# Performance work log

Hardware: AMD Instinct MI355X
Metric: run time of the kernel (lower is better)

## Reference

```python
import jax, jax.numpy as jnp
import numpy as np

N_NODES = 16384
K_NBR = 16
N_HOPS = 4  # hops + 2
IN_DIM = 256
RAW_DIM = 128
OUT_DIM = 64
PHI_DIM = 16
N_KERN = 4
E = N_NODES * K_NBR


def setup_inputs() -> dict:
    key = jax.random.key(0)
    ks = jax.random.split(key, 16)
    s = 0.05  # small weight scale for numerical sanity
    h = jax.random.normal(ks[0], (N_NODES, IN_DIM), jnp.float32)
    e_tensor = jax.random.normal(ks[1], (N_HOPS, N_NODES, RAW_DIM), jnp.float32)
    # kNN-style edges: each dst node has exactly K_NBR incoming edges
    src = jax.random.randint(ks[2], (N_HOPS, E), 0, N_NODES, jnp.int32)
    dst = jnp.tile(jnp.repeat(jnp.arange(N_NODES, dtype=jnp.int32), K_NBR)[None, :], (N_HOPS, 1))
    return {
        'h': h,
        'e_tensor': e_tensor,
        'src': src,
        'dst': dst,
        'W_phi': jax.random.normal(ks[3], (N_HOPS, RAW_DIM, PHI_DIM - 1), jnp.float32) * s,
        'mlp_w1': jax.random.normal(ks[4], (N_HOPS, RAW_DIM, IN_DIM), jnp.float32) * s,
        'mlp_b1': jax.random.normal(ks[5], (N_HOPS, IN_DIM), jnp.float32) * s,
        'mlp_w2': jax.random.normal(ks[6], (N_HOPS, IN_DIM, PHI_DIM * N_KERN), jnp.float32) * s,
        'mlp_b2': jax.random.normal(ks[7], (N_HOPS, PHI_DIM * N_KERN), jnp.float32) * s,
        'tilde_phi': jax.random.normal(ks[8], (N_HOPS, N_KERN, PHI_DIM), jnp.float32),
        'W': jax.random.normal(ks[9], (N_HOPS, IN_DIM, OUT_DIM * N_KERN), jnp.float32) * s,
        'bias': jax.random.normal(ks[10], (N_HOPS, OUT_DIM), jnp.float32) * s,
        'z': jax.random.normal(ks[11], (OUT_DIM, 1), jnp.float32),
    }


def _deform_gconv(h, e_l, src, dst, W_phi, w1, b1, w2, b2, tilde_phi, W, bias):
    N = h.shape[0]
    nk, phi_dim = tilde_phi.shape
    hk = (h @ W).reshape(N, nk, -1)                                  # (N, nk, out)
    phi = e_l @ W_phi                                                # (N, phi-1)
    tn = tilde_phi / jnp.linalg.norm(tilde_phi, axis=1, keepdims=True)  # (nk, phi)
    hid = jax.nn.relu(e_l @ w1 + b1)
    delta = (hid @ w2 + b2).reshape(N, nk, phi_dim)                  # (N, nk, phi)
    delta_ik = tn[None, :, :] + delta                                # (N, nk, phi)
    # per-edge quantities (edges carry dst-node delta_ik, u_sub_v distance)
    dist = phi[src] - phi[dst]                                       # (E, phi-1)
    last = jnp.all(dist == 0, axis=1, keepdims=True).astype(dist.dtype)
    dist = jnp.concatenate([dist, last], axis=1)                     # (E, phi)
    dist = dist / jnp.maximum(jnp.linalg.norm(dist, axis=1, keepdims=True), 1e-8)
    logits = jnp.einsum('ep,ekp->ek', dist, delta_ik[dst])           # (E, nk)
    # edge_softmax over incoming edges of each dst node
    mx = jax.ops.segment_max(logits, dst, num_segments=N)
    ex = jnp.exp(logits - mx[dst])
    den = jax.ops.segment_sum(ex, dst, num_segments=N)
    att = ex / den[dst]                                              # (E, nk)
    # message passing: m = h[src] * att, sum over incoming edges
    m = hk[src] * att[:, :, None]                                    # (E, nk, out)
    agg = jax.ops.segment_sum(m, dst, num_segments=N)                # (N, nk, out)
    out = agg.sum(1) + bias[None, :]
    out = out / jnp.maximum(jnp.linalg.norm(out, axis=1, keepdims=True), 1e-8)
    # regularizers
    d = tn[:, None, :] - tn[None, :, :]                              # (nk, nk, phi)
    l_sep = jnp.sum(jnp.sum(d * d, axis=-1)) / nk                    # sum_i mean_j ||t_i - t_j||^2
    l_focus = jnp.mean(jnp.sum(delta * delta, axis=2))
    return out, l_sep, l_focus


def reference(h, e_tensor, src, dst, W_phi, mlp_w1, mlp_b1, mlp_w2, mlp_b2, tilde_phi, W, bias, z):
    outs, l_seps, l_fos = jax.vmap(
        _deform_gconv, in_axes=(None, 0, 0, 0, 0, 0, 0, 0, 0, 0, 0, 0)
    )(h, e_tensor, src, dst, W_phi, mlp_w1, mlp_b1, mlp_w2, mlp_b2, tilde_phi, W, bias)
    # hop-level softmax fusion
    score = jnp.einsum('hno,oz->hnz', outs, z)                       # (n_hops, N, 1)
    att = jax.nn.softmax(score, axis=0)
    tilde_h = jnp.sum(att * outs, axis=0)                            # (N, out)
    l_sep = jnp.mean(l_seps)
    l_focus = jnp.mean(l_fos)
    return tilde_h, l_sep, l_focus
```

## Files before the change

kernel.cpp:

```cpp
#include <hip/hip_runtime.h>
#include <hip/hip_bf16.h>

#define N_NODES 16384
#define K_NBR 16
#define HOPS 4
#define IN_DIM 256
#define RAW_DIM 128
#define OUT_DIM 64
#define PHI_DIM 16
#define N_KERN 4
#define E_EDGES (N_NODES * K_NBR)

typedef __hip_bfloat16 bf16;
typedef __attribute__((ext_vector_type(8))) short short8;
typedef __attribute__((ext_vector_type(4))) float f32x4;
typedef __attribute__((ext_vector_type(2))) float f32x2;
typedef __attribute__((ext_vector_type(4))) unsigned int uint4v;

__device__ __forceinline__ float toF(float x) { return x; }
__device__ __forceinline__ float toF(bf16 x) { return __bfloat162float(x); }
__device__ __forceinline__ short f2bfbits(float f)
{
    bf16 b = __float2bfloat16(f);
    short s; __builtin_memcpy(&s, &b, 2); return s;
}

#define SWZ(row, colShort) ((colShort) ^ (((row) & 7) << 3))
#define SWZ32(row, colShort) ((colShort) ^ ((((row) >> 1) & 3) << 3))

__device__ __forceinline__ void gld_lds16(const bf16* g, short* l)
{
    __builtin_amdgcn_global_load_lds(
        (const __attribute__((address_space(1))) unsigned int*)g,
        (__attribute__((address_space(3))) unsigned int*)l, 16, 0, 0);
}

template <int IMM>
__device__ __forceinline__ float swzx(float v)
{
    return __builtin_bit_cast(float,
        __builtin_amdgcn_ds_swizzle(__builtin_bit_cast(int, v), IMM));
}
#define XOR1  0x041F
#define XOR2  0x081F
#define XOR4  0x101F
#define XOR8  0x201F
#define XOR16 0x401F

__device__ __forceinline__ void pkfma_w0(f32x2& acc, f32x2 w, f32x2 x)
{
    asm("v_pk_fma_f32 %0, %1, %2, %0 op_sel:[0,0,0] op_sel_hi:[0,1,1]"
        : "+v"(acc) : "v"(w), "v"(x));
}
__device__ __forceinline__ void pkfma_w1(f32x2& acc, f32x2 w, f32x2 x)
{
    asm("v_pk_fma_f32 %0, %1, %2, %0 op_sel:[1,0,0] op_sel_hi:[1,1,1]"
        : "+v"(acc) : "v"(w), "v"(x));
}

#define CVC_B1   0
#define CVC_B2   (CVC_B1 + HOPS * IN_DIM)
#define CVC_BIAS (CVC_B2 + HOPS * PHI_DIM * N_KERN)
#define CVC_Z    (CVC_BIAS + HOPS * OUT_DIM)
#define CVC_END  (CVC_Z + OUT_DIM)

#define WT_N  (HOPS * 256 * 256)
#define W1T_N (HOPS * 256 * 128)
#define W2T_N (HOPS * 64 * 256)
#define WPT_N (HOPS * 16 * 128)
#define CVT_TOTAL (WT_N + W1T_N + W2T_N + WPT_N)

#define NB_CV ((CVC_END + 255) / 256)
#define NB_WT (CVT_TOTAL / 1024)
#define NB_H  (N_NODES * 256 / 8 / 2048)
#define NB_E  (HOPS * N_NODES * 128 / 8 / 2048)
#define NB_ALL (NB_CV + NB_WT + NB_H + NB_E + 1)

#define GA_TOTAL 2048

__device__ __forceinline__ float loadDyn(const void* p, int i, bool isbf)
{
    return isbf ? toF(((const bf16*)p)[i]) : ((const float*)p)[i];
}

__device__ __forceinline__ void cvt8(bf16* dst, const void* src, size_t base, bool isbf)
{
    short8 v;
    if (isbf) {
        v = *(const short8*)((const bf16*)src + base);
    } else {
        const float* sp = (const float*)src + base;
        f32x4 f0 = *(const f32x4*)sp;
        f32x4 f1 = *(const f32x4*)(sp + 4);
#pragma unroll
        for (int j = 0; j < 4; j++) { v[j] = f2bfbits(f0[j]); v[4 + j] = f2bfbits(f1[j]); }
    }
    *(short8*)(dst + base) = v;
}

__global__ __launch_bounds__(256) void cvt_all(
    const void* h, const void* e,
    const void* wphi, const void* w1, const void* b1, const void* w2,
    const void* b2, const void* tphi, const void* W, const void* bias,
    const void* z, float* __restrict__ CV,
    bf16* __restrict__ wt, bf16* __restrict__ w1t, bf16* __restrict__ w2t,
    bf16* __restrict__ wpt, bf16* __restrict__ h_bf, bf16* __restrict__ e_bf,
    float* __restrict__ tn_out, float* __restrict__ acc, int* __restrict__ flagOut)
{
    __shared__ float s_det[4];
    int tid = threadIdx.x;
    {
        unsigned short pv = ((const unsigned short*)h)[tid];
        unsigned int bits = ((unsigned int)pv) << 16;
        float v; __builtin_memcpy(&v, &bits, 4);
        v = fabsf(v);
        if (!(v == v) || v > 1e30f) v = 1e30f;
#pragma unroll
        for (int off = 32; off > 0; off >>= 1) v = fmaxf(v, __shfl_xor(v, off));
        if ((tid & 63) == 0) s_det[tid >> 6] = v;
    }
    __syncthreads();
    bool isbf = fmaxf(fmaxf(s_det[0], s_det[1]), fmaxf(s_det[2], s_det[3])) < 1e4f;

    int b = blockIdx.x;
    if (b == NB_ALL - 1) {
        __shared__ float s_v[256], s_tn[256], s_red[256], s_hop[4];
        int hop = tid >> 6, t64 = tid & 63;
        int row = t64 >> 4, p = t64 & 15;
        float v = loadDyn(tphi, hop * 64 + t64, isbf);
        s_v[tid] = v;
        __syncthreads();
        float ss = 0.f;
        for (int q = 0; q < 16; q++) { float x = s_v[hop * 64 + row * 16 + q]; ss += x * x; }
        float tnv = v / sqrtf(ss);
        tn_out[hop * 64 + t64] = tnv;
        s_tn[tid] = tnv;
        __syncthreads();
        float s = 0.f;
        for (int j = 0; j < 4; j++) {
            float d = tnv - s_tn[hop * 64 + j * 16 + p];
            s += d * d;
        }
        s_red[tid] = s;
        __syncthreads();
        if (t64 == 0) {
            float tot = 0.f;
            for (int i = 0; i < 64; i++) tot += s_red[hop * 64 + i];
            s_hop[hop] = tot;
        }
        __syncthreads();
        if (tid == 0) {
            acc[0] = (s_hop[0] + s_hop[1] + s_hop[2] + s_hop[3]) * 0.0625f;
            acc[1] = 0.f;
            *flagOut = isbf ? 1 : 0;
        }
        return;
    }
    if (b < NB_CV) {
        int idx = b * 256 + tid;
        if (idx >= CVC_END) return;
        float v;
        if      (idx < CVC_B2)   v = loadDyn(b1,   idx - CVC_B1,   isbf);
        else if (idx < CVC_BIAS) v = loadDyn(b2,   idx - CVC_B2,   isbf);
        else if (idx < CVC_Z)    v = loadDyn(bias, idx - CVC_BIAS, isbf);
        else                     v = loadDyn(z,    idx - CVC_Z,    isbf);
        CV[idx] = v;
        return;
    }
    b -= NB_CV;
    if (b < NB_WT) {
        int base = (b * 256 + tid) * 4;
#pragma unroll
        for (int jj = 0; jj < 4; jj++) {
            int idx = base + jj;
            if (idx < WT_N) {
                int o = idx, hop = o >> 16, rem = o & 65535, n = rem >> 8, k = rem & 255;
                wt[o] = __float2bfloat16(loadDyn(W, hop * 65536 + k * 256 + n, isbf));
            } else if (idx < WT_N + W1T_N) {
                int o = idx - WT_N, hop = o >> 15, rem = o & 32767, n = rem >> 7, k = rem & 127;
                w1t[o] = __float2bfloat16(loadDyn(w1, hop * 32768 + k * 256 + n, isbf));
            } else if (idx < WT_N + W1T_N + W2T_N) {
                int o = idx - WT_N - W1T_N, hop = o >> 14, rem = o & 16383, n = rem >> 8, k = rem & 255;
                w2t[o] = __float2bfloat16(loadDyn(w2, hop * 16384 + k * 64 + n, isbf));
            } else {
                int o = idx - WT_N - W1T_N - W2T_N, hop = o >> 11, rem = o & 2047, n = rem >> 7, k = rem & 127;
                float v = (n < 15) ? loadDyn(wphi, hop * 1920 + k * 15 + n, isbf) : 0.f;
                wpt[o] = __float2bfloat16(v);
            }
        }
        return;
    }
    b -= NB_WT;
    if (b < NB_H) {
#pragma unroll
        for (int k = 0; k < 8; k++) {
            size_t base = ((size_t)b * 2048 + k * 256 + tid) * 8;
            cvt8(h_bf, h, base, isbf);
        }
        return;
    }
    b -= NB_H;
    {
#pragma unroll
        for (int k = 0; k < 8; k++) {
            size_t base = ((size_t)b * 2048 + k * 256 + tid) * 8;
            cvt8(e_bf, e, base, isbf);
        }
    }
}

__device__ __forceinline__ void gemm_hk_dev(
    char* smem, const bf16* __restrict__ A, const bf16* __restrict__ Bt,
    unsigned char* __restrict__ Cg, int colBase, int rowBase)
{
    short* base = (short*)smem;
    int tid = threadIdx.x;
    int w = tid >> 6, lane = tid & 63;
    int wr = w >> 1, wc = w & 1;
    int l16 = lane & 15, quad = lane >> 4;
    f32x4 acc[4][4] = {};

#define HK_STAGE(bufb, k0v)                                                          \
    {                                                                                \
        short* As_ = base + (bufb) * 8192;                                           \
        short* Bs_ = As_ + 4096;                                                     \
        for (int id = tid; id < 128 * 4; id += 256) {                                \
            int row = id >> 2, j = id & 3;                                           \
            gld_lds16(A + (size_t)(rowBase + row) * 256 + (k0v) +                    \
                          ((j ^ ((row >> 1) & 3)) * 8),                              \
                      As_ + id * 8);                                                 \
        }                                                                            \
        for (int id = tid; id < 128 * 4; id += 256) {                                \
            int row = id >> 2, j = id & 3;                                           \
            gld_lds16(Bt + (size_t)(colBase + row) * 256 + (k0v) +                   \
                          ((j ^ ((row >> 1) & 3)) * 8),                              \
                      Bs_ + id * 8);                                                 \
        }                                                                            \
    }

    HK_STAGE(0, 0)
    __syncthreads();
    for (int t = 0; t < 8; ++t) {
        if (t < 7) HK_STAGE((t + 1) & 1, (t + 1) * 32)
        short* As = base + (t & 1) * 8192;
        short* Bs = As + 4096;
        short8 aF[4], bF[4];
#pragma unroll
        for (int mi = 0; mi < 4; mi++) {
            int row = wr * 64 + mi * 16 + l16;
            aF[mi] = *(const short8*)&As[row * 32 + SWZ32(row, quad * 8)];
        }
#pragma unroll
        for (int ni = 0; ni < 4; ni++) {
            int row = wc * 64 + ni * 16 + l16;
            bF[ni] = *(const short8*)&Bs[row * 32 + SWZ32(row, quad * 8)];
        }
#pragma unroll
        for (int mi = 0; mi < 4; mi++)
#pragma unroll
            for (int ni = 0; ni < 4; ni++)
                acc[mi][ni] = __builtin_amdgcn_mfma_f32_16x16x32_bf16(
                    aF[mi], bF[ni], acc[mi][ni], 0, 0, 0);
        __syncthreads();
    }
#undef HK_STAGE

    unsigned char* Cs = (unsigned char*)smem;
#pragma unroll
    for (int mi = 0; mi < 4; mi++)
#pragma unroll
        for (int ni = 0; ni < 4; ni++) {
            int cl = wc * 64 + ni * 16 + l16;
#pragma unroll
            for (int r = 0; r < 4; r++) {
                int rl = wr * 64 + mi * 16 + quad * 4 + r;
                float v = acc[mi][ni][r];
                int pk = __builtin_amdgcn_cvt_pk_fp8_f32(v, v, 0, false);
                Cs[rl * 128 + cl] = (unsigned char)(pk & 0xFF);
            }
        }
    __syncthreads();
    for (int c = tid; c < 128 * 8; c += 256) {
        int r = c >> 3, off = (c & 7) * 16;
        *(uint4v*)(Cg + ((size_t)(rowBase + r) * 256 + colBase) + off) =
            *(const uint4v*)(Cs + (size_t)r * 128 + off);
    }
}

__device__ __forceinline__ void hid_delta_dev(
    char* smem,
    const bf16* __restrict__ A, const bf16* __restrict__ B1,
    const bf16* __restrict__ B2, const bf16* __restrict__ WP,
    const float* __restrict__ b1, const float* __restrict__ b2,
    const float* __restrict__ tn, float* __restrict__ Dg,
    float* __restrict__ phiG, float* __restrict__ lfocus, int rowBase)
{
    short* As  = (short*)smem;
    short* Bs  = As + 64 * 64;
    short* Wpa = As + 20480;
    short* Hs  = (short*)smem;
    short* B2s = Hs + 64 * 256;
    float* Ds  = (float*)smem;
    float* s_w = (float*)(smem + 40944);

    int tid = threadIdx.x;
    int w = tid >> 6, lane = tid & 63;
    int l16 = lane & 15, quad = lane >> 4;

    {
        f32x4 acc[4][4] = {};
        f32x4 accp[4] = {};
        for (int k0 = 0; k0 < 128; k0 += 64) {
            for (int id = tid; id < 64 * 8; id += 256) {
                int row = id >> 3, j = id & 7;
                gld_lds16(A + (size_t)(rowBase + row) * 128 + k0 + ((j ^ (row & 7)) * 8),
                          As + id * 8);
            }
            for (int id = tid; id < 256 * 8; id += 256) {
                int row = id >> 3, j = id & 7;
                gld_lds16(B1 + (size_t)row * 128 + k0 + ((j ^ (row & 7)) * 8),
                          Bs + id * 8);
            }
            if (k0 == 0) {
                int row = tid >> 4, j = tid & 15;
                gld_lds16(WP + (size_t)row * 128 + ((j ^ (row & 7)) * 8),
                          Wpa + tid * 8);
            }
            __syncthreads();
#pragma unroll
            for (int kc = 0; kc < 64; kc += 32) {
                short8 aF[4], bF[4];
#pragma unroll
                for (int mi = 0; mi < 4; mi++) {
                    int row = mi * 16 + l16;
                    aF[mi] = *(const short8*)&As[row * 64 + SWZ(row, kc + quad * 8)];
                }
#pragma unroll
                for (int ni = 0; ni < 4; ni++) {
                    int row = w * 64 + ni * 16 + l16;
                    bF[ni] = *(const short8*)&Bs[row * 64 + SWZ(row, kc + quad * 8)];
                }
#pragma unroll
                for (int mi = 0; mi < 4; mi++)
#pragma unroll
                    for (int ni = 0; ni < 4; ni++)
                        acc[mi][ni] = __builtin_amdgcn_mfma_f32_16x16x32_bf16(
                            aF[mi], bF[ni], acc[mi][ni], 0, 0, 0);
                if (w == 0) {
                    short8 bFp = *(const short8*)&Wpa[l16 * 128 + SWZ(l16, k0 + kc + quad * 8)];
#pragma unroll
                    for (int mi = 0; mi < 4; mi++)
                        accp[mi] = __builtin_amdgcn_mfma_f32_16x16x32_bf16(
                            aF[mi], bFp, accp[mi], 0, 0, 0);
                }
            }
            __syncthreads();
        }
#pragma unroll
        for (int mi = 0; mi < 4; mi++) {
#pragma unroll
            for (int ni = 0; ni < 4; ni++) {
                int col = w * 64 + ni * 16 + l16;
                float bv = b1[col];
#pragma unroll
                for (int r = 0; r < 4; r++) {
                    int row = mi * 16 + quad * 4 + r;
                    float v = fmaxf(acc[mi][ni][r] + bv, 0.f);
                    Hs[row * 256 + SWZ(row, col)] = f2bfbits(v);
                }
            }
        }
        for (int id = tid; id < 64 * 8; id += 256) {
            int row = id >> 3, j = id & 7;
            gld_lds16(B2 + (size_t)row * 256 + ((j ^ (row & 7)) * 8),
                      B2s + id * 8);
        }
        if (w == 0) {
#pragma unroll
            for (int mi = 0; mi < 4; mi++)
#pragma unroll
                for (int r = 0; r < 4; r++)
                    phiG[(size_t)(rowBase + mi * 16 + quad * 4 + r) * 16 + l16] =
                        accp[mi][r];
        }
    }

    {
        f32x4 acc2[4] = {};
        for (int q = 0; q < 4; q++) {
            __syncthreads();
#pragma unroll
            for (int kcq = 0; kcq < 64; kcq += 32) {
                int arow = w * 16 + l16;
                short8 aF = *(const short8*)&Hs[arow * 256 + SWZ(arow, q * 64 + kcq + quad * 8)];
                short8 bF[4];
#pragma unroll
                for (int ni = 0; ni < 4; ni++) {
                    int row = ni * 16 + l16;
                    bF[ni] = *(const short8*)&B2s[row * 64 + SWZ(row, kcq + quad * 8)];
                }
#pragma unroll
                for (int ni = 0; ni < 4; ni++)
                    acc2[ni] = __builtin_amdgcn_mfma_f32_16x16x32_bf16(aF, bF[ni], acc2[ni], 0, 0, 0);
            }
            if (q < 3) {
                __syncthreads();
                for (int id = tid; id < 64 * 8; id += 256) {
                    int row = id >> 3, j = id & 7;
                    gld_lds16(B2 + (size_t)row * 256 + (q + 1) * 64 + ((j ^ (row & 7)) * 8),
                              B2s + id * 8);
                }
            }
        }
        __syncthreads();
        float sq = 0.f;
#pragma unroll
        for (int ni = 0; ni < 4; ni++) {
            int col = ni * 16 + l16;
            float bv = b2[col], tv = tn[col];
#pragma unroll
            for (int r = 0; r < 4; r++) {
                int row = w * 16 + quad * 4 + r;
                float v = acc2[ni][r] + bv;
                sq += v * v;
                Ds[row * 64 + col] = v + tv;
            }
        }
#pragma unroll
        for (int off = 32; off > 0; off >>= 1) sq += __shfl_xor(sq, off);
        if (lane == 0) s_w[w] = sq;
        __syncthreads();
        for (int c = tid; c < 64 * 16; c += 256) {
            int r = c >> 4, off = (c & 15) * 4;
            *(uint4v*)(Dg + (size_t)(rowBase + r) * 64 + off) =
                *(const uint4v*)(Ds + (size_t)r * 64 + off);
        }
        if (tid == 0) atomicAdd(lfocus, s_w[0] + s_w[1] + s_w[2] + s_w[3]);
    }
}

__global__ __launch_bounds__(256) void gemm_all(
    const bf16* __restrict__ h_bf, const bf16* __restrict__ e_bf,
    const bf16* __restrict__ WT, const bf16* __restrict__ WPT,
    const bf16* __restrict__ W1T, const bf16* __restrict__ W2T,
    const float* __restrict__ b1All, const float* __restrict__ b2All,
    const float* __restrict__ tnAll, unsigned char* __restrict__ hk_f8,
    float* __restrict__ phi, float* __restrict__ DELTA, float* __restrict__ lfocus)
{
    __shared__ __align__(16) char smem[45056];
    int b = blockIdx.x;
    int x = b & 7;
    int p = b >> 3;
    int s = p >> 1;
    if ((p & 1) == 0) {
        int rg = x * 16 + (s >> 3);
        int v = s & 7;
        int hop = v >> 1, part = v & 1;
        gemm_hk_dev(smem, h_bf, WT + (size_t)hop * 65536,
                    hk_f8 + (size_t)hop * N_NODES * 256, part * 128, rg * 128);
    } else {
        int hop = x & 3;
        int tile = ((x >> 2) << 7) + s;
        hid_delta_dev(smem,
            e_bf + (size_t)hop * N_NODES * 128,
            W1T + (size_t)hop * 32768, W2T + (size_t)hop * 16384,
            WPT + (size_t)hop * 2048,
            b1All + hop * 256, b2All + hop * 64, tnAll + hop * 64,
            DELTA + (size_t)hop * N_NODES * 64,
            phi + (size_t)hop * N_NODES * 16, lfocus, tile * 64);
    }
}

__global__ __launch_bounds__(256) void edge_agg2(
    const unsigned char* __restrict__ hk, const float* __restrict__ phi,
    const float* __restrict__ dik, const int* __restrict__ src,
    const float* __restrict__ biasAll, float* __restrict__ outs)
{
    int b = blockIdx.x;
    int hop = b & 3;
    int wave = threadIdx.x >> 6, lane = threadIdx.x & 63;
    int node = (b >> 2) * 4 + wave;
    const unsigned char* hk_l = hk + (size_t)hop * N_NODES * 256;
    const float* phi_l  = phi + (size_t)hop * N_NODES * 16;
    const float* dik_l  = dik + (size_t)hop * N_NODES * 64;
    const int*   src_n  = src + (size_t)hop * E_EDGES + (size_t)node * 16;
    const float* bias_l = biasAll + hop * 64;
    float*       outs_n = outs + ((size_t)hop * N_NODES + node) * 64;

    __shared__ __align__(16) float s_dik[4][64];
    __shared__ __align__(16) float s_attT[4][4][24];
    __shared__ int   s_src[4][16];

    s_dik[wave][lane] = dik_l[(size_t)node * 64 + lane];
    if (lane < 16) s_src[wave][lane] = src_n[lane];

    int e = lane >> 2, q = lane & 3;
    int sN = s_src[wave][e];
    f32x4 ps = *(const f32x4*)(phi_l + (size_t)sN * 16 + q * 4);
    f32x4 pd = *(const f32x4*)(phi_l + (size_t)node * 16 + q * 4);
    float d0 = ps[0] - pd[0], d1 = ps[1] - pd[1];
    float d2 = ps[2] - pd[2], d3 = ps[3] - pd[3];
    bool q3 = (q == 3);
    float ssp = d0 * d0 + d1 * d1 + d2 * d2 + (q3 ? 0.f : d3 * d3);
    ssp += swzx<XOR1>(ssp); ssp += swzx<XOR2>(ssp);
    float last = (ssp == 0.f) ? 1.f : 0.f;
    if (q3) d3 = last;
    float inv = fminf(__builtin_amdgcn_rsqf(ssp + last * last), 1e8f);
#pragma unroll
    for (int k = 0; k < 4; k++) {
        f32x4 dkv = *(const f32x4*)&s_dik[wave][k * 16 + q * 4];
        float pk = d0 * dkv[0] + d1 * dkv[1] + d2 * dkv[2] + d3 * dkv[3];
        pk += swzx<XOR1>(pk); pk += swzx<XOR2>(pk);
        if (q == k) s_attT[wave][k][e] = pk * inv;
    }

    int k2 = lane & 3;
    float lgv = s_attT[wave][k2][e];
    float mx = lgv;
    mx = fmaxf(mx, swzx<XOR4>(mx));
    mx = fmaxf(mx, swzx<XOR8>(mx));
    mx = fmaxf(mx, swzx<XOR16>(mx));
    mx = fmaxf(mx, __shfl_xor(mx, 32));
    float ex = __expf(lgv - mx);
    float den = ex;
    den += swzx<XOR4>(den);
    den += swzx<XOR8>(den);
    den += swzx<XOR16>(den);
    den += __shfl_xor(den, 32);
    s_attT[wave][k2][e] = ex * __builtin_amdgcn_rcpf(den);

    int kk = lane >> 4, dsub = (lane & 15) * 4;
    f32x2 att2[8];
#pragma unroll
    for (int g = 0; g < 8; g++) att2[g] = *(const f32x2*)&s_attT[wave][kk][g * 2];
    f32x2 a01 = {0.f, 0.f}, a23 = {0.f, 0.f};
#pragma unroll
    for (int ep = 0; ep < 8; ep++) {
        int sm0 = __builtin_amdgcn_readfirstlane(s_src[wave][2 * ep]);
        int sm1 = __builtin_amdgcn_readfirstlane(s_src[wave][2 * ep + 1]);
        unsigned int u0 = *(const unsigned int*)(hk_l + (size_t)sm0 * 256 + lane * 4);
        unsigned int u1 = *(const unsigned int*)(hk_l + (size_t)sm1 * 256 + lane * 4);
        f32x2 w = att2[ep];
        pkfma_w0(a01, w, __builtin_amdgcn_cvt_pk_f32_fp8((int)u0, false));
        pkfma_w0(a23, w, __builtin_amdgcn_cvt_pk_f32_fp8((int)u0, true));
        pkfma_w1(a01, w, __builtin_amdgcn_cvt_pk_f32_fp8((int)u1, false));
        pkfma_w1(a23, w, __builtin_amdgcn_cvt_pk_f32_fp8((int)u1, true));
    }
    float a0 = a01[0], a1 = a01[1], a2 = a23[0], a3 = a23[1];
    a0 += swzx<XOR16>(a0); a0 += __shfl_xor(a0, 32);
    a1 += swzx<XOR16>(a1); a1 += __shfl_xor(a1, 32);
    a2 += swzx<XOR16>(a2); a2 += __shfl_xor(a2, 32);
    a3 += swzx<XOR16>(a3); a3 += __shfl_xor(a3, 32);
    f32x4 bv = *(const f32x4*)(bias_l + dsub);
    float o0 = a0 + bv[0];
    float o1 = a1 + bv[1];
    float o2 = a2 + bv[2];
    float o3 = a3 + bv[3];
    float ssq = o0 * o0 + o1 * o1 + o2 * o2 + o3 * o3;
    ssq += swzx<XOR1>(ssq);
    ssq += swzx<XOR2>(ssq);
    ssq += swzx<XOR4>(ssq);
    ssq += swzx<XOR8>(ssq);
    float inv2 = fminf(__builtin_amdgcn_rsqf(ssq), 1e8f);
    if (kk == 0) {
        f32x4 st;
        st[0] = o0 * inv2; st[1] = o1 * inv2; st[2] = o2 * inv2; st[3] = o3 * inv2;
        *(f32x4*)(outs_n + dsub) = st;
    }
}

__global__ __launch_bounds__(256) void fuse_kernel(
    const float* __restrict__ outs, const float* __restrict__ z,
    void* __restrict__ out, const int* __restrict__ flag,
    const float* __restrict__ acc)
{
    int tid = threadIdx.x;
    int node = blockIdx.x * 4 + (tid >> 6);
    int dd = tid & 63;
    float zv = z[dd];
    float o[4], sc[4];
#pragma unroll
    for (int h = 0; h < 4; h++) {
        o[h] = outs[((size_t)h * N_NODES + node) * 64 + dd];
        float v = o[h] * zv;
#pragma unroll
        for (int off = 32; off > 0; off >>= 1) v += __shfl_xor(v, off);
        sc[h] = v;
    }
    float mx = fmaxf(fmaxf(sc[0], sc[1]), fmaxf(sc[2], sc[3]));
    float e0 = __expf(sc[0] - mx), e1 = __expf(sc[1] - mx);
    float e2 = __expf(sc[2] - mx), e3 = __expf(sc[3] - mx);
    float den = e0 + e1 + e2 + e3;
    float t = (e0 * o[0] + e1 * o[1] + e2 * o[2] + e3 * o[3]) * __builtin_amdgcn_rcpf(den);
    size_t oi = (size_t)node * 64 + dd;
    bool isbf = (*flag != 0);
    if (isbf) ((bf16*)out)[oi] = __float2bfloat16(t);
    else      ((float*)out)[oi] = t;
    if (blockIdx.x == 0 && tid == 0) {
        float a = acc[0];
        float b = acc[1] / ((float)N_NODES * 4.f * 4.f);
        size_t base = (size_t)N_NODES * 64;
        if (isbf) {
            ((bf16*)out)[base]     = __float2bfloat16(a);
            ((bf16*)out)[base + 1] = __float2bfloat16(b);
        } else {
            ((float*)out)[base]     = a;
            ((float*)out)[base + 1] = b;
        }
    }
}

extern "C" void kernel_launch(void* const* d_in, const int* in_sizes, int n_in,
                              void* d_out, int out_size, void* d_ws, size_t ws_size,
                              hipStream_t stream)
{
    const void* h    = d_in[0];
    const void* e    = d_in[1];
    const int*  src  = (const int*)d_in[2];
    const void* Wphi = d_in[4];
    const void* w1   = d_in[5];
    const void* b1   = d_in[6];
    const void* w2   = d_in[7];
    const void* b2   = d_in[8];
    const void* tphi = d_in[9];
    const void* W    = d_in[10];
    const void* bias = d_in[11];
    const void* z    = d_in[12];

    float* ws    = (float*)d_ws;
    float* CV    = ws;
    float* OUTS  = CV + CVC_END;
    float* PHI   = OUTS + (size_t)4 * N_NODES * 64;
    float* DELTA = PHI + (size_t)4 * N_NODES * 16;
    float* TN    = DELTA + (size_t)4 * N_NODES * 64;
    float* ACC   = TN + 256;
    int*   FLAG  = (int*)(ACC + 2);
    bf16*  H_BF  = (bf16*)(ACC + 4);
    bf16*  E_BF  = H_BF + (size_t)N_NODES * 256;
    bf16*  WT    = E_BF + (size_t)HOPS * N_NODES * 128;
    bf16*  W1T   = WT + WT_N;
    bf16*  W2T   = W1T + W1T_N;
    bf16*  WPT   = W2T + W2T_N;
    unsigned char* HK_F8 = (unsigned char*)(WPT + WPT_N);

    cvt_all<<<NB_ALL, 256, 0, stream>>>(
        h, e, Wphi, w1, b1, w2, b2, tphi, W, bias, z, CV,
        WT, W1T, W2T, WPT, H_BF, E_BF, TN, ACC, FLAG);

    gemm_all<<<dim3(GA_TOTAL), 256, 0, stream>>>(
        H_BF, E_BF, WT, WPT, W1T, W2T,
        CV + CVC_B1, CV + CVC_B2, TN, HK_F8, PHI, DELTA, ACC + 1);

    edge_agg2<<<dim3(N_NODES), 256, 0, stream>>>(
        HK_F8, PHI, DELTA, src, CV + CVC_BIAS, OUTS);

    fuse_kernel<<<dim3(N_NODES / 4), 256, 0, stream>>>(
        OUTS, CV + CVC_Z, d_out, FLAG, ACC);
}
```

Measured before the change: 194.8 us.

## Deepen K-tiles and hand-schedule LDS pipeline in fused GEMM kernel

The hk GEMM now uses 64-wide K tiles (4 iterations instead of 8) with double buffering, explicit vmcnt/lgkmcnt waits and raw s_barrier so global-to-LDS loads of the next stage overlap MFMA work. The hid/delta second GEMM loads all of W2 into LDS at once, removing three reload/sync rounds. Shared memory grows to 64 KB and launch bounds request 2 blocks per CU, which may lower occupancy and relies on hand-counted waitcnt values being correct.

New measurement: 195.6 us. About the same (+0.4%).

```diff
diff --git a/kernel.cpp b/kernel.cpp
--- a/kernel.cpp
+++ b/kernel.cpp
@@ -26,7 +26,6 @@
 }
 
 #define SWZ(row, colShort) ((colShort) ^ (((row) & 7) << 3))
-#define SWZ32(row, colShort) ((colShort) ^ ((((row) >> 1) & 3) << 3))
 
 __device__ __forceinline__ void gld_lds16(const bf16* g, short* l)
 {
@@ -222,46 +221,65 @@
 
 #define HK_STAGE(bufb, k0v)                                                          \
     {                                                                                \
-        short* As_ = base + (bufb) * 8192;                                           \
-        short* Bs_ = As_ + 4096;                                                     \
-        for (int id = tid; id < 128 * 4; id += 256) {                                \
-            int row = id >> 2, j = id & 3;                                           \
-            gld_lds16(A + (size_t)(rowBase + row) * 256 + (k0v) +                    \
-                          ((j ^ ((row >> 1) & 3)) * 8),                              \
+        short* As_ = base + (bufb) * 16384;                                          \
+        short* Bs_ = As_ + 8192;                                                     \
+        for (int id = tid; id < 128 * 8; id += 256) {                                \
+            int row = id >> 3, j = id & 7;                                           \
+            gld_lds16(A + (size_t)(rowBase + row) * 256 + (k0v) + ((j ^ (row & 7)) * 8), \
                       As_ + id * 8);                                                 \
         }                                                                            \
-        for (int id = tid; id < 128 * 4; id += 256) {                                \
-            int row = id >> 2, j = id & 3;                                           \
-            gld_lds16(Bt + (size_t)(colBase + row) * 256 + (k0v) +                   \
-                          ((j ^ ((row >> 1) & 3)) * 8),                              \
+        for (int id = tid; id < 128 * 8; id += 256) {                                \
+            int row = id >> 3, j = id & 7;                                           \
+            gld_lds16(Bt + (size_t)(colBase + row) * 256 + (k0v) + ((j ^ (row & 7)) * 8), \
                       Bs_ + id * 8);                                                 \
         }                                                                            \
     }
 
     HK_STAGE(0, 0)
-    __syncthreads();
-    for (int t = 0; t < 8; ++t) {
-        if (t < 7) HK_STAGE((t + 1) & 1, (t + 1) * 32)
-        short* As = base + (t & 1) * 8192;
-        short* Bs = As + 4096;
-        short8 aF[4], bF[4];
-#pragma unroll
-        for (int mi = 0; mi < 4; mi++) {
-            int row = wr * 64 + mi * 16 + l16;
-            aF[mi] = *(const short8*)&As[row * 32 + SWZ32(row, quad * 8)];
-        }
-#pragma unroll
-        for (int ni = 0; ni < 4; ni++) {
-            int row = wc * 64 + ni * 16 + l16;
-            bF[ni] = *(const short8*)&Bs[row * 32 + SWZ32(row, quad * 8)];
-        }
-#pragma unroll
-        for (int mi = 0; mi < 4; mi++)
-#pragma unroll
-            for (int ni = 0; ni < 4; ni++)
-                acc[mi][ni] = __builtin_amdgcn_mfma_f32_16x16x32_bf16(
-                    aF[mi], bF[ni], acc[mi][ni], 0, 0, 0);
-        __syncthreads();
+    HK_STAGE(1, 64)
+    asm volatile("s_waitcnt vmcnt(8)" ::: "memory");
+    __builtin_amdgcn_sched_barrier(0);
+    __builtin_amdgcn_s_barrier();
+    __builtin_amdgcn_sched_barrier(0);
+#pragma unroll
+    for (int t = 0; t < 4; ++t) {
+        short* As = base + (t & 1) * 16384;
+        short* Bs = As + 8192;
+        short8 aF[2][4], bF[2][4];
+#pragma unroll
+        for (int hh = 0; hh < 2; hh++) {
+            int kc = hh * 32;
+#pragma unroll
+            for (int mi = 0; mi < 4; mi++) {
+                int row = wr * 64 + mi * 16 + l16;
+                aF[hh][mi] = *(const short8*)&As[row * 64 + SWZ(row, kc + quad * 8)];
+            }
+#pragma unroll
+            for (int ni = 0; ni < 4; ni++) {
+                int row = wc * 64 + ni * 16 + l16;
+                bF[hh][ni] = *(const short8*)&Bs[row * 64 + SWZ(row, kc + quad * 8)];
+            }
+        }
+        asm volatile("s_waitcnt lgkmcnt(0)" ::: "memory");
+        __builtin_amdgcn_sched_barrier(0);
+        __builtin_amdgcn_s_barrier();
+        __builtin_amdgcn_sched_barrier(0);
+        if (t < 2) HK_STAGE(t & 1, (t + 2) * 64)
+#pragma unroll
+        for (int hh = 0; hh < 2; hh++)
+#pragma unroll
+            for (int mi = 0; mi < 4; mi++)
+#pragma unroll
+                for (int ni = 0; ni < 4; ni++)
+                    acc[mi][ni] = __builtin_amdgcn_mfma_f32_16x16x32_bf16(
+                        aF[hh][mi], bF[hh][ni], acc[mi][ni], 0, 0, 0);
+        if (t < 3) {
+            if (t < 2) { asm volatile("s_waitcnt vmcnt(8)" ::: "memory"); }
+            else       { asm volatile("s_waitcnt vmcnt(0)" ::: "memory"); }
+            __builtin_amdgcn_sched_barrier(0);
+            __builtin_amdgcn_s_barrier();
+            __builtin_amdgcn_sched_barrier(0);
+        }
     }
 #undef HK_STAGE
 
@@ -296,12 +314,12 @@
     float* __restrict__ phiG, float* __restrict__ lfocus, int rowBase)
 {
     short* As  = (short*)smem;
-    short* Bs  = As + 64 * 64;
+    short* Bs  = As + 4096;
     short* Wpa = As + 20480;
     short* Hs  = (short*)smem;
-    short* B2s = Hs + 64 * 256;
+    short* B2s = Hs + 16384;
     float* Ds  = (float*)smem;
-    float* s_w = (float*)(smem + 40944);
+    float* s_w = (float*)(smem + 65520);
 
     int tid = threadIdx.x;
     int w = tid >> 6, lane = tid & 63;
@@ -370,8 +388,8 @@
                 }
             }
         }
-        for (int id = tid; id < 64 * 8; id += 256) {
-            int row = id >> 3, j = id & 7;
+        for (int id = tid; id < 64 * 32; id += 256) {
+            int row = id >> 5, j = id & 31;
             gld_lds16(B2 + (size_t)row * 256 + ((j ^ (row & 7)) * 8),
                       B2s + id * 8);
         }
@@ -386,33 +404,27 @@
     }
 
     {
+        __syncthreads();
         f32x4 acc2[4] = {};
-        for (int q = 0; q < 4; q++) {
-            __syncthreads();
-#pragma unroll
-            for (int kcq = 0; kcq < 64; kcq += 32) {
-                int arow = w * 16 + l16;
-                short8 aF = *(const short8*)&Hs[arow * 256 + SWZ(arow, q * 64 + kcq + quad * 8)];
-                short8 bF[4];
-#pragma unroll
-                for (int ni = 0; ni < 4; ni++) {
-                    int row = ni * 16 + l16;
-                    bF[ni] = *(const short8*)&B2s[row * 64 + SWZ(row, kcq + quad * 8)];
-                }
-#pragma unroll
-                for (int ni = 0; ni < 4; ni++)
-                    acc2[ni] = __builtin_amdgcn_mfma_f32_16x16x32_bf16(aF, bF[ni], acc2[ni], 0, 0, 0);
-            }
-            if (q < 3) {
-                __syncthreads();
-                for (int id = tid; id < 64 * 8; id += 256) {
-                    int row = id >> 3, j = id & 7;
-                    gld_lds16(B2 + (size_t)row * 256 + (q + 1) * 64 + ((j ^ (row & 7)) * 8),
-                              B2s + id * 8);
-                }
-            }
-        }
-        __syncthreads();
+        int arow = w * 16 + l16;
+#pragma unroll
+        for (int q = 0; q < 8; q++) {
+            int kc = q * 32;
+            short8 aF = *(const short8*)&Hs[arow * 256 + SWZ(arow, kc + quad * 8)];
+            short8 bFq[4];
+#pragma unroll
+            for (int ni = 0; ni < 4; ni++) {
+                int brow = ni * 16 + l16;
+                bFq[ni] = *(const short8*)&B2s[brow * 256 + SWZ(brow, kc + quad * 8)];
+            }
+#pragma unroll
+            for (int ni = 0; ni < 4; ni++)
+                acc2[ni] = __builtin_amdgcn_mfma_f32_16x16x32_bf16(aF, bFq[ni], acc2[ni], 0, 0, 0);
+        }
+        asm volatile("s_waitcnt lgkmcnt(0)" ::: "memory");
+        __builtin_amdgcn_sched_barrier(0);
+        __builtin_amdgcn_s_barrier();
+        __builtin_amdgcn_sched_barrier(0);
         float sq = 0.f;
 #pragma unroll
         for (int ni = 0; ni < 4; ni++) {
@@ -439,7 +451,7 @@
     }
 }
 
-__global__ __launch_bounds__(256) void gemm_all(
+__global__ __launch_bounds__(256, 2) void gemm_all(
     const bf16* __restrict__ h_bf, const bf16* __restrict__ e_bf,
     const bf16* __restrict__ WT, const bf16* __restrict__ WPT,
     const bf16* __restrict__ W1T, const bf16* __restrict__ W2T,
@@ -447,7 +459,7 @@
     const float* __restrict__ tnAll, unsigned char* __restrict__ hk_f8,
     float* __restrict__ phi, float* __restrict__ DELTA, float* __restrict__ lfocus)
 {
-    __shared__ __align__(16) char smem[45056];
+    __shared__ __align__(16) char smem[65536];
     int b = blockIdx.x;
     int x = b & 7;
     int p = b >> 3;
```
